# Performance work log

Measured on AMD Instinct MI355X. Metric: run time of the kernel, lower is better.

The kernel has to match this reference:

```python
import jax, jax.numpy as jnp
import numpy as np

B, D, I = 16384, 2048, 2048


def setup_inputs() -> dict:
    key = jax.random.key(0)
    kx, kh, kw = jax.random.split(key, 3)
    x = jax.random.normal(kx, (B, I), dtype=jnp.float32)
    h = jax.random.normal(kh, (B, D), dtype=jnp.float32)
    # input projection weight (Linear, no bias): [d_model, inpt_size]
    W_ih = jax.random.normal(kw, (D, I), dtype=jnp.float32) * 0.02
    # orthogonal-ish hidden transition (torch uses an SVD-orthogonal block),
    # well-conditioned so the inverse is exact and stable
    rng = np.random.default_rng(0)
    q, _ = np.linalg.qr(rng.standard_normal((D, D)).astype(np.float64))
    W_hh = jnp.asarray(q, dtype=jnp.float32)
    W_inv = jnp.asarray(np.linalg.inv(q), dtype=jnp.float32)  # buffer self.inv
    return {"x": x, "h": h, "W_ih": W_ih, "W_hh": W_hh, "W_inv": W_inv}


def reference(x, h, W_ih, W_hh, W_inv):
    # outs = inpt_linear(x) : [B, D]
    outs = jnp.einsum("bi,di->bd", x, W_ih)
    not_trig = outs[..., -1] >= -1.0          # [B]
    h_last = h[..., -1]                        # [B]
    m_fwd = ((h_last > 0) & not_trig)[..., None]   # forward rotation branch
    m_inv = ((h_last < 0) & not_trig)[..., None]   # inverse rotation branch
    m_pass = (~not_trig)[..., None]                # passthrough branch
    hW = h @ W_hh   # torch.matmul(h, weight_hh) (no transpose)
    hI = h @ W_inv  # torch.matmul(h, inv)
    zero = jnp.zeros((), dtype=outs.dtype)
    return (outs
            + jnp.where(m_fwd, hW, zero)
            + jnp.where(m_inv, hI, zero)
            + jnp.where(m_pass, h, zero))
```

## Files before the change

kernel.cpp:

```cpp
#include <hip/hip_runtime.h>
#include <hip/hip_bf16.h>
#include <stdint.h>

#define B_ROWS 16384
#define DIM 2048
#define BK 64
#define NT 96

typedef float f32x4 __attribute__((ext_vector_type(4)));
typedef short bf16x8 __attribute__((ext_vector_type(8)));
using u16 = unsigned short;
using u32 = unsigned int;

__device__ __forceinline__ u32 pack_bf2(float a, float b) {
  __hip_bfloat162 t = __float22bfloat162_rn(float2{a, b});
  union { __hip_bfloat162 b2; u32 u; } cv;
  cv.b2 = t;
  return cv.u;
}

__device__ __forceinline__ u16 f2bf_rne(float f) {
  union { float f; u32 u; } v;
  v.f = f;
  u32 u = v.u;
  u32 r = u + 0x7FFFu + ((u >> 16) & 1u);
  return (u16)(r >> 16);
}

__device__ __forceinline__ void gload16(const void* g, void* l) {
  __builtin_amdgcn_global_load_lds(
      (const __attribute__((address_space(1))) u32*)g,
      (__attribute__((address_space(3))) u32*)l, 16, 0, 0);
}

__global__ __launch_bounds__(256) void k_prep(
    const float* __restrict__ x, const float* __restrict__ h,
    const float* __restrict__ W_ih, int* __restrict__ flags,
    u16* __restrict__ xb, u16* __restrict__ hF, u16* __restrict__ hI) {
  int row = blockIdx.x * 4 + (threadIdx.x >> 6);
  int lane = threadIdx.x & 63;
  const float* xr = x + (size_t)row * DIM;
  const float* hr = h + (size_t)row * DIM;
  const float* wr = W_ih + (size_t)(DIM - 1) * DIM;
  u16* xbr = xb + (size_t)row * DIM;
  double s = 0.0;
  u32 hp[16];
#pragma unroll
  for (int i = 0; i < 8; ++i) {
    int idx = (i * 64 + lane) * 4;
    f32x4 xv = *(const f32x4*)(xr + idx);
    f32x4 wv = *(const f32x4*)(wr + idx);
    f32x4 hv = *(const f32x4*)(hr + idx);
    s += (double)xv.x * wv.x + (double)xv.y * wv.y +
         (double)xv.z * wv.z + (double)xv.w * wv.w;
    *(uint2*)(xbr + idx) = uint2{pack_bf2(xv.x, xv.y), pack_bf2(xv.z, xv.w)};
    hp[2 * i] = pack_bf2(hv.x, hv.y);
    hp[2 * i + 1] = pack_bf2(hv.z, hv.w);
  }
#pragma unroll
  for (int off = 32; off > 0; off >>= 1) s += __shfl_xor(s, off);
  float hl = hr[DIM - 1];
  int f = (s < -1.0) ? 2 : (hl > 0.f ? 0 : (hl < 0.f ? 1 : 3));
  if (lane == 0) flags[row] = f;
  uint2 z{0u, 0u};
  u16* hFr = hF + (size_t)row * DIM;
  u16* hIr = hI + (size_t)row * DIM;
#pragma unroll
  for (int i = 0; i < 8; ++i) {
    int idx = (i * 64 + lane) * 4;
    uint2 p{hp[2 * i], hp[2 * i + 1]};
    *(uint2*)(hFr + idx) = (f == 0) ? p : z;
    *(uint2*)(hIr + idx) = (f == 1) ? p : z;
  }
}

__global__ __launch_bounds__(256) void k_flags_fb(
    const float* __restrict__ x, const float* __restrict__ h,
    const float* __restrict__ W_ih, int* __restrict__ flags) {
  int row = blockIdx.x * 4 + (threadIdx.x >> 6);
  int lane = threadIdx.x & 63;
  const float* xr = x + (size_t)row * DIM;
  const float* wr = W_ih + (size_t)(DIM - 1) * DIM;
  double s = 0.0;
#pragma unroll
  for (int i = 0; i < 8; ++i) {
    int idx = (i * 64 + lane) * 4;
    f32x4 xv = *(const f32x4*)(xr + idx);
    f32x4 wv = *(const f32x4*)(wr + idx);
    s += (double)xv.x * wv.x + (double)xv.y * wv.y +
         (double)xv.z * wv.z + (double)xv.w * wv.w;
  }
#pragma unroll
  for (int off = 32; off > 0; off >>= 1) s += __shfl_xor(s, off);
  if (lane == 0) {
    float hl = h[(size_t)row * DIM + (DIM - 1)];
    flags[row] = (s < -1.0) ? 2 : (hl > 0.f ? 0 : (hl < 0.f ? 1 : 3));
  }
}

__global__ __launch_bounds__(256) void k_convert(const float* __restrict__ src,
                                                 u16* __restrict__ dst) {
  size_t i = ((size_t)blockIdx.x * 256 + threadIdx.x) * 4;
  f32x4 v = *(const f32x4*)(src + i);
  *(uint2*)(dst + i) = uint2{pack_bf2(v.x, v.y), pack_bf2(v.z, v.w)};
}

__global__ __launch_bounds__(256) void k_transpose(const float* __restrict__ src,
                                                   u16* __restrict__ dst) {
  __shared__ float tile[32][33];
  int k0 = blockIdx.x * 32;
  int n0 = blockIdx.y * 32;
  int tx = threadIdx.x & 31;
  int ty = threadIdx.x >> 5;
#pragma unroll
  for (int i = 0; i < 4; ++i)
    tile[ty + 8 * i][tx] = src[(size_t)(k0 + ty + 8 * i) * DIM + n0 + tx];
  __syncthreads();
#pragma unroll
  for (int i = 0; i < 4; ++i)
    dst[(size_t)(n0 + ty + 8 * i) * DIM + k0 + tx] = f2bf_rne(tile[tx][ty + 8 * i]);
}

__global__ __launch_bounds__(512, 2) void k_gemm8(
    const u16* __restrict__ xb, const u16* __restrict__ hF,
    const u16* __restrict__ hI, const u16* __restrict__ Wih,
    const u16* __restrict__ WhhT, const u16* __restrict__ WinvT,
    const int* __restrict__ flags, const float* __restrict__ h,
    float* __restrict__ out) {
  __shared__ __attribute__((aligned(128))) char smem[131072];

  int o = blockIdx.x;
  int swz = (o & 7) * 64 + (o >> 3);
  int brow = (swz >> 3) * 256;
  int bcol = (swz & 7) * 256;

  int t = threadIdx.x;
  int lane = t & 63;
  int wave = t >> 6;
  int wr = wave >> 2;
  int wc = wave & 3;

  int sx16 = (((lane & 3) ^ ((lane >> 3) & 3)) << 4);
  int fA = (((lane >> 4) ^ ((lane >> 1) & 3)) << 4);
  int arowbase = wr * 128 + (lane & 15);
  int browbase = wc * 64 + (lane & 15);

  auto stage = [&](int T, int isB, int kk) {
    if (T >= NT) T -= NT;
    int seg = T >> 5;
    int kt = T & 31;
    const u16* mat = isB ? (seg == 0 ? Wih : seg == 1 ? WhhT : WinvT)
                         : (seg == 0 ? xb : seg == 1 ? hF : hI);
    int r0 = isB ? bcol : brow;
    size_t gb = (size_t)(r0 + wave * 32 + (lane >> 2)) * (DIM * 2) +
                (size_t)kt * 128 + (size_t)kk * 64 + (size_t)sx16;
    char* ldst = smem + ((T & 1) << 16) + kk * 32768 + isB * 16384 +
                 (wave * 32) * 64;
    gload16((const char*)mat + gb, ldst);
    gload16((const char*)mat + gb + (size_t)16 * (DIM * 2), ldst + 1024);
  };

  f32x4 acc[8][4] = {};
  bf16x8 aF[8], bF[4];

  stage(0, 0, 0); stage(0, 1, 0);
  stage(0, 0, 1); stage(0, 1, 1);
  stage(1, 0, 0); stage(1, 1, 0);
  asm volatile("s_waitcnt vmcnt(8)" ::: "memory");
  __builtin_amdgcn_s_barrier();

#define PHASE(KK, STT, STKK)                                                   \
  {                                                                            \
    const char* Ab_ = smem + buf + (KK) * 32768;                               \
    _Pragma("unroll") for (int m = 0; m < 4; ++m) {                            \
      aF[m] = *(const bf16x8*)(Ab_ + (arowbase + m * 16) * 64 + fA);           \
      aF[4 + m] = *(const bf16x8*)(Ab_ + (arowbase + 64 + m * 16) * 64 + fA);  \
    }                                                                          \
    _Pragma("unroll") for (int n = 0; n < 4; ++n)                              \
        bF[n] = *(const bf16x8*)(Ab_ + 16384 + (browbase + n * 16) * 64 + fA); \
    stage(STT, 0, STKK);                                                       \
    stage(STT, 1, STKK);                                                       \
    asm volatile("s_waitcnt vmcnt(8)" ::: "memory");                           \
    __builtin_amdgcn_s_barrier();                                              \
    asm volatile("s_waitcnt lgkmcnt(0)" ::: "memory");                         \
    __builtin_amdgcn_sched_barrier(0);                                         \
    __builtin_amdgcn_s_setprio(1);                                             \
    _Pragma("unroll") for (int mh = 0; mh < 2; ++mh)                           \
        _Pragma("unroll") for (int m = 0; m < 4; ++m)                          \
            _Pragma("unroll") for (int n = 0; n < 4; ++n)                      \
                acc[mh * 4 + m][n] = __builtin_amdgcn_mfma_f32_16x16x32_bf16(  \
                    aF[mh * 4 + m], bF[n], acc[mh * 4 + m][n], 0, 0, 0);       \
    __builtin_amdgcn_s_setprio(0);                                             \
  }

#pragma unroll 1
  for (int T = 0; T < NT; ++T) {
    const int buf = (T & 1) << 16;
    PHASE(0, T + 1, 1)
    PHASE(1, T + 2, 0)
  }
#undef PHASE
  asm volatile("s_waitcnt vmcnt(0)" ::: "memory");

#pragma unroll
  for (int mi = 0; mi < 8; ++mi) {
    int rbase = brow + wr * 128 + (mi >> 2) * 64 + (mi & 3) * 16 + (lane >> 4) * 4;
#pragma unroll
    for (int j = 0; j < 4; ++j) {
      int row = rbase + j;
      bool pass = (flags[row] == 2);
#pragma unroll
      for (int n = 0; n < 4; ++n) {
        int col = bcol + wc * 64 + n * 16 + (lane & 15);
        float v = acc[mi][n][j];
        if (pass) v += h[(size_t)row * DIM + col];
        out[(size_t)row * DIM + col] = v;
      }
    }
  }
}

#define BM 128
#define BN 128
__global__ __launch_bounds__(256, 2) void k_gemm_fb(
    const float* __restrict__ x, const float* __restrict__ h,
    const u16* __restrict__ Wih, const u16* __restrict__ WhhT,
    const u16* __restrict__ WinvT, const int* __restrict__ flags,
    float* __restrict__ out) {
  __shared__ char smem[(BM + BN) * BK * 2];
  char* sA = smem;
  char* sB = smem + BM * BK * 2;

  int o = blockIdx.x;
  int swz = (o & 7) * ((int)gridDim.x >> 3) + (o >> 3);
  int brow = (swz >> 4) * BM;
  int bcol = (swz & 15) * BN;

  int t = threadIdx.x;
  int lane = t & 63;
  int wave = t >> 6;
  int wrow = (wave >> 1) * 64;
  int wcol = (wave & 1) * 64;

  f32x4 acc[4][4] = {};
  int sc = t & 15;
  int sr0 = t >> 4;

  int aOff[4][2], bOff[4][2];
#pragma unroll
  for (int m = 0; m < 4; ++m)
#pragma unroll
    for (int kk = 0; kk < 2; ++kk) {
      int ar = wrow + m * 16 + (lane & 15);
      aOff[m][kk] = ar * (BK * 2) + ((kk * 64 + (lane >> 4) * 16) ^ ((ar & 7) << 4));
      int br = wcol + m * 16 + (lane & 15);
      bOff[m][kk] = br * (BK * 2) + ((kk * 64 + (lane >> 4) * 16) ^ ((br & 7) << 4));
    }

#pragma unroll 1
  for (int seg = 0; seg < 3; ++seg) {
    const float* Asrc = (seg == 0) ? x : h;
    const u16* Bsrc = (seg == 0) ? Wih : (seg == 1) ? WhhT : WinvT;
    int want = seg - 1;

    float rmask[8];
#pragma unroll
    for (int i = 0; i < 8; ++i) {
      int r = sr0 + 16 * i;
      rmask[i] = (want < 0 || flags[brow + r] == want) ? 1.f : 0.f;
    }

#pragma unroll 1
    for (int k0 = 0; k0 < DIM; k0 += BK) {
      __syncthreads();
#pragma unroll
      for (int i = 0; i < 8; ++i) {
        int r = sr0 + 16 * i;
        f32x4 v = *(const f32x4*)(Asrc + (size_t)(brow + r) * DIM + k0 + sc * 4);
        float msk = rmask[i];
        int off = r * (BK * 2) + ((sc * 8) ^ ((r & 7) << 4));
        *(uint2*)(sA + off) =
            uint2{pack_bf2(v.x * msk, v.y * msk), pack_bf2(v.z * msk, v.w * msk)};
      }
#pragma unroll
      for (int i = 0; i < 4; ++i) {
        int ch = t + 256 * i;
        int r = ch >> 3;
        int c = ch & 7;
        uint4 v = *(const uint4*)(Bsrc + (size_t)(bcol + r) * DIM + k0 + c * 8);
        int off = r * (BK * 2) + ((c * 16) ^ ((r & 7) << 4));
        *(uint4*)(sB + off) = v;
      }
      __syncthreads();
      bf16x8 aF2[4][2], bF2[4][2];
#pragma unroll
      for (int m = 0; m < 4; ++m)
#pragma unroll
        for (int kk = 0; kk < 2; ++kk) {
          aF2[m][kk] = *(const bf16x8*)(sA + aOff[m][kk]);
          bF2[m][kk] = *(const bf16x8*)(sB + bOff[m][kk]);
        }
#pragma unroll
      for (int kk = 0; kk < 2; ++kk)
#pragma unroll
        for (int m = 0; m < 4; ++m)
#pragma unroll
          for (int n = 0; n < 4; ++n)
            acc[m][n] = __builtin_amdgcn_mfma_f32_16x16x32_bf16(
                aF2[m][kk], bF2[n][kk], acc[m][n], 0, 0, 0);
    }
  }

#pragma unroll
  for (int m = 0; m < 4; ++m) {
    int rbase = brow + wrow + m * 16 + (lane >> 4) * 4;
#pragma unroll
    for (int j = 0; j < 4; ++j) {
      int row = rbase + j;
      bool pass = (flags[row] == 2);
#pragma unroll
      for (int n = 0; n < 4; ++n) {
        int col = bcol + wcol + n * 16 + (lane & 15);
        float v = acc[m][n][j];
        if (pass) v += h[(size_t)row * DIM + col];
        out[(size_t)row * DIM + col] = v;
      }
    }
  }
}

extern "C" void kernel_launch(void* const* d_in, const int* in_sizes, int n_in,
                              void* d_out, int out_size, void* d_ws, size_t ws_size,
                              hipStream_t stream) {
  const float* x = (const float*)d_in[0];
  const float* h = (const float*)d_in[1];
  const float* W_ih = (const float*)d_in[2];
  const float* W_hh = (const float*)d_in[3];
  const float* W_inv = (const float*)d_in[4];
  float* out = (float*)d_out;

  char* ws = (char*)d_ws;
  int* flags = (int*)ws;
  u16* WihB = (u16*)(ws + (64 << 10));
  u16* WhhT = WihB + (size_t)DIM * DIM;
  u16* WinvT = WhhT + (size_t)DIM * DIM;
  u16* xb = WinvT + (size_t)DIM * DIM;
  u16* hF = xb + (size_t)B_ROWS * DIM;
  u16* hI = hF + (size_t)B_ROWS * DIM;
  size_t need = (size_t)(64 << 10) + 3ull * DIM * DIM * 2 + 3ull * B_ROWS * DIM * 2;

  k_convert<<<(DIM * DIM / 4) / 256, 256, 0, stream>>>(W_ih, WihB);
  k_transpose<<<dim3(DIM / 32, DIM / 32), 256, 0, stream>>>(W_hh, WhhT);
  k_transpose<<<dim3(DIM / 32, DIM / 32), 256, 0, stream>>>(W_inv, WinvT);

  if (ws_size >= need) {
    k_prep<<<B_ROWS / 4, 256, 0, stream>>>(x, h, W_ih, flags, xb, hF, hI);
    k_gemm8<<<(B_ROWS / 256) * (DIM / 256), 512, 0, stream>>>(
        xb, hF, hI, WihB, WhhT, WinvT, flags, h, out);
  } else {
    k_flags_fb<<<B_ROWS / 4, 256, 0, stream>>>(x, h, W_ih, flags);
    k_gemm_fb<<<(B_ROWS / BM) * (DIM / BN), 256, 0, stream>>>(x, h, WihB, WhhT,
                                                              WinvT, flags, out);
  }
}
```

Before: 503.2 us.

## Double-buffer MFMA operand fragments in registers to overlap LDS reads with compute

Replaces the single aF/bF fragment set with two register sets (rfA/rfB) that alternate per half-step. Each phase now issues the LDS reads for the next phase's operands and then runs MFMAs on fragments loaded in the previous phase. The old full lgkmcnt(0) wait before the MFMAs becomes a partial lgkmcnt(12) wait, and the global-load wait is tightened to vmcnt(4) to match the new prefetch distance. The aim is to hide LDS latency behind matrix math. The cost is higher VGPR pressure, which could reduce occupancy or cause spills, plus more delicate hazard ordering between the register prefetch and the LDS buffer refills.

```diff
diff --git a/kernel.cpp b/kernel.cpp
--- a/kernel.cpp
+++ b/kernel.cpp
@@ -161,45 +161,60 @@
   };
 
   f32x4 acc[8][4] = {};
-  bf16x8 aF[8], bF[4];
+  bf16x8 rfA[12], rfB[12];
 
   stage(0, 0, 0); stage(0, 1, 0);
   stage(0, 0, 1); stage(0, 1, 1);
   stage(1, 0, 0); stage(1, 1, 0);
-  asm volatile("s_waitcnt vmcnt(8)" ::: "memory");
+  asm volatile("s_waitcnt vmcnt(4)" ::: "memory");
   __builtin_amdgcn_s_barrier();
-
-#define PHASE(KK, STT, STKK)                                                   \
+#pragma unroll
+  for (int m = 0; m < 4; ++m) {
+    rfA[m] = *(const bf16x8*)(smem + (arowbase + m * 16) * 64 + fA);
+    rfA[4 + m] = *(const bf16x8*)(smem + (arowbase + 64 + m * 16) * 64 + fA);
+  }
+#pragma unroll
+  for (int n = 0; n < 4; ++n)
+    rfB[8 + n] = rfA[8 + n] = *(const bf16x8*)(smem + 16384 +
+                                               (browbase + n * 16) * 64 + fA);
+#pragma unroll
+  for (int n = 0; n < 4; ++n)
+    rfA[8 + n] = *(const bf16x8*)(smem + 16384 + (browbase + n * 16) * 64 + fA);
+
+#define PHASEBODY(RFUSE, RFLOAD, NB, ST1, SKK)                                 \
   {                                                                            \
-    const char* Ab_ = smem + buf + (KK) * 32768;                               \
+    const char* nb_ = (NB);                                                    \
     _Pragma("unroll") for (int m = 0; m < 4; ++m) {                            \
-      aF[m] = *(const bf16x8*)(Ab_ + (arowbase + m * 16) * 64 + fA);           \
-      aF[4 + m] = *(const bf16x8*)(Ab_ + (arowbase + 64 + m * 16) * 64 + fA);  \
+      RFLOAD[m] = *(const bf16x8*)(nb_ + (arowbase + m * 16) * 64 + fA);       \
+      RFLOAD[4 + m] =                                                          \
+          *(const bf16x8*)(nb_ + (arowbase + 64 + m * 16) * 64 + fA);          \
     }                                                                          \
     _Pragma("unroll") for (int n = 0; n < 4; ++n)                              \
-        bF[n] = *(const bf16x8*)(Ab_ + 16384 + (browbase + n * 16) * 64 + fA); \
-    stage(STT, 0, STKK);                                                       \
-    stage(STT, 1, STKK);                                                       \
-    asm volatile("s_waitcnt vmcnt(8)" ::: "memory");                           \
+        RFLOAD[8 + n] =                                                        \
+            *(const bf16x8*)(nb_ + 16384 + (browbase + n * 16) * 64 + fA);     \
+    stage(ST1, 0, SKK);                                                        \
+    stage(ST1, 1, SKK);                                                        \
+    asm volatile("s_waitcnt lgkmcnt(12)" ::: "memory");                        \
+    asm volatile("s_waitcnt vmcnt(4)" ::: "memory");                           \
     __builtin_amdgcn_s_barrier();                                              \
-    asm volatile("s_waitcnt lgkmcnt(0)" ::: "memory");                         \
     __builtin_amdgcn_sched_barrier(0);                                         \
     __builtin_amdgcn_s_setprio(1);                                             \
     _Pragma("unroll") for (int mh = 0; mh < 2; ++mh)                           \
         _Pragma("unroll") for (int m = 0; m < 4; ++m)                          \
             _Pragma("unroll") for (int n = 0; n < 4; ++n)                      \
                 acc[mh * 4 + m][n] = __builtin_amdgcn_mfma_f32_16x16x32_bf16(  \
-                    aF[mh * 4 + m], bF[n], acc[mh * 4 + m][n], 0, 0, 0);       \
+                    RFUSE[mh * 4 + m], RFUSE[8 + n], acc[mh * 4 + m][n],       \
+                    0, 0, 0);                                                  \
     __builtin_amdgcn_s_setprio(0);                                             \
   }
 
 #pragma unroll 1
   for (int T = 0; T < NT; ++T) {
-    const int buf = (T & 1) << 16;
-    PHASE(0, T + 1, 1)
-    PHASE(1, T + 2, 0)
-  }
-#undef PHASE
+    const int b = (T & 1) << 16;
+    PHASEBODY(rfA, rfB, smem + b + 32768, T + 1, 1)
+    PHASEBODY(rfB, rfA, smem + (b ^ 65536), T + 2, 0)
+  }
+#undef PHASEBODY
   asm volatile("s_waitcnt vmcnt(0)" ::: "memory");
 
 #pragma unroll
```

Result: slower. 517.1 us (+2.8%).

## Sort rows by branch flag so each GEMM tile computes only its needed matmul

Applied to the files above, without the earlier changes.

Rows are grouped by branch (forward, inverse, passthrough) using a single-block scan that builds a permutation. Each group is padded to 256-row tiles and packed into bf16 buffers. Each GEMM tile then runs K=4096 (x·Wih plus h·Whh or h·Winv) or only K=2048 for passthrough tiles, instead of always running K=6144 with zeroed h copies. The cost is extra kernels (flags, a serial scan, a permute gather), padding waste, and scattered output writes through the permutation.

```diff
diff --git a/kernel.cpp b/kernel.cpp
--- a/kernel.cpp
+++ b/kernel.cpp
@@ -5,7 +5,7 @@
 #define B_ROWS 16384
 #define DIM 2048
 #define BK 64
-#define NT 96
+#define MAXPR 17152
 
 typedef float f32x4 __attribute__((ext_vector_type(4)));
 typedef short bf16x8 __attribute__((ext_vector_type(8)));
@@ -33,48 +33,7 @@
       (__attribute__((address_space(3))) u32*)l, 16, 0, 0);
 }
 
-__global__ __launch_bounds__(256) void k_prep(
-    const float* __restrict__ x, const float* __restrict__ h,
-    const float* __restrict__ W_ih, int* __restrict__ flags,
-    u16* __restrict__ xb, u16* __restrict__ hF, u16* __restrict__ hI) {
-  int row = blockIdx.x * 4 + (threadIdx.x >> 6);
-  int lane = threadIdx.x & 63;
-  const float* xr = x + (size_t)row * DIM;
-  const float* hr = h + (size_t)row * DIM;
-  const float* wr = W_ih + (size_t)(DIM - 1) * DIM;
-  u16* xbr = xb + (size_t)row * DIM;
-  double s = 0.0;
-  u32 hp[16];
-#pragma unroll
-  for (int i = 0; i < 8; ++i) {
-    int idx = (i * 64 + lane) * 4;
-    f32x4 xv = *(const f32x4*)(xr + idx);
-    f32x4 wv = *(const f32x4*)(wr + idx);
-    f32x4 hv = *(const f32x4*)(hr + idx);
-    s += (double)xv.x * wv.x + (double)xv.y * wv.y +
-         (double)xv.z * wv.z + (double)xv.w * wv.w;
-    *(uint2*)(xbr + idx) = uint2{pack_bf2(xv.x, xv.y), pack_bf2(xv.z, xv.w)};
-    hp[2 * i] = pack_bf2(hv.x, hv.y);
-    hp[2 * i + 1] = pack_bf2(hv.z, hv.w);
-  }
-#pragma unroll
-  for (int off = 32; off > 0; off >>= 1) s += __shfl_xor(s, off);
-  float hl = hr[DIM - 1];
-  int f = (s < -1.0) ? 2 : (hl > 0.f ? 0 : (hl < 0.f ? 1 : 3));
-  if (lane == 0) flags[row] = f;
-  uint2 z{0u, 0u};
-  u16* hFr = hF + (size_t)row * DIM;
-  u16* hIr = hI + (size_t)row * DIM;
-#pragma unroll
-  for (int i = 0; i < 8; ++i) {
-    int idx = (i * 64 + lane) * 4;
-    uint2 p{hp[2 * i], hp[2 * i + 1]};
-    *(uint2*)(hFr + idx) = (f == 0) ? p : z;
-    *(uint2*)(hIr + idx) = (f == 1) ? p : z;
-  }
-}
-
-__global__ __launch_bounds__(256) void k_flags_fb(
+__global__ __launch_bounds__(256) void k_flags(
     const float* __restrict__ x, const float* __restrict__ h,
     const float* __restrict__ W_ih, int* __restrict__ flags) {
   int row = blockIdx.x * 4 + (threadIdx.x >> 6);
@@ -98,6 +57,82 @@
   }
 }
 
+__global__ __launch_bounds__(256) void k_scan(const int* __restrict__ flags,
+                                              int* __restrict__ iperm,
+                                              int* __restrict__ meta) {
+  __shared__ int sF[257], sI[257], sP[257];
+  int t = threadIdx.x;
+  int cF = 0, cI = 0, cP = 0;
+  for (int i = 0; i < 64; ++i) {
+    int f = flags[t * 64 + i];
+    cF += (f == 0); cI += (f == 1); cP += (f >= 2);
+  }
+  sF[t + 1] = cF; sI[t + 1] = cI; sP[t + 1] = cP;
+  for (int i = t; i < MAXPR; i += 256) iperm[i] = -1;
+  __syncthreads();
+  if (t == 0) {
+    sF[0] = sI[0] = sP[0] = 0;
+    for (int i = 1; i <= 256; ++i) {
+      sF[i] += sF[i - 1]; sI[i] += sI[i - 1]; sP[i] += sP[i - 1];
+    }
+  }
+  __syncthreads();
+  int totF = sF[256], totI = sI[256], totP = sP[256];
+  int padF = (totF + 255) & ~255;
+  int padI = (totI + 255) & ~255;
+  int rowsFI = padF + padI;
+  int nrows = rowsFI + totP;
+  if (t == 0) {
+    meta[0] = (nrows + 255) >> 8;
+    meta[1] = rowsFI >> 8;
+    meta[2] = rowsFI;
+    meta[3] = padF;
+  }
+  int oF = sF[t], oI = padF + sI[t], oP = rowsFI + sP[t];
+  for (int i = 0; i < 64; ++i) {
+    int r = t * 64 + i;
+    int f = flags[r];
+    if (f == 0) iperm[oF++] = r;
+    else if (f == 1) iperm[oI++] = r;
+    else iperm[oP++] = r;
+  }
+}
+
+__global__ __launch_bounds__(256) void k_permute(
+    const float* __restrict__ x, const float* __restrict__ h,
+    const int* __restrict__ iperm, const int* __restrict__ meta,
+    u16* __restrict__ xP, u16* __restrict__ hP) {
+  int p = blockIdx.x * 4 + (threadIdx.x >> 6);
+  int lane = threadIdx.x & 63;
+  int rowsFI = meta[2];
+  int orig = iperm[p];
+  u16* xpr = xP + (size_t)p * DIM;
+  u16* hpr = hP + (size_t)p * DIM;
+  bool doH = p < rowsFI;
+  if (orig >= 0) {
+    const float* xr = x + (size_t)orig * DIM;
+    const float* hr = h + (size_t)orig * DIM;
+#pragma unroll
+    for (int i = 0; i < 8; ++i) {
+      int idx = (i * 64 + lane) * 4;
+      f32x4 xv = *(const f32x4*)(xr + idx);
+      *(uint2*)(xpr + idx) = uint2{pack_bf2(xv.x, xv.y), pack_bf2(xv.z, xv.w)};
+      if (doH) {
+        f32x4 hv = *(const f32x4*)(hr + idx);
+        *(uint2*)(hpr + idx) = uint2{pack_bf2(hv.x, hv.y), pack_bf2(hv.z, hv.w)};
+      }
+    }
+  } else {
+    uint2 z{0u, 0u};
+#pragma unroll
+    for (int i = 0; i < 8; ++i) {
+      int idx = (i * 64 + lane) * 4;
+      *(uint2*)(xpr + idx) = z;
+      if (doH) *(uint2*)(hpr + idx) = z;
+    }
+  }
+}
+
 __global__ __launch_bounds__(256) void k_convert(const float* __restrict__ src,
                                                  u16* __restrict__ dst) {
   size_t i = ((size_t)blockIdx.x * 256 + threadIdx.x) * 4;
@@ -122,17 +157,25 @@
 }
 
 __global__ __launch_bounds__(512, 2) void k_gemm8(
-    const u16* __restrict__ xb, const u16* __restrict__ hF,
-    const u16* __restrict__ hI, const u16* __restrict__ Wih,
-    const u16* __restrict__ WhhT, const u16* __restrict__ WinvT,
-    const int* __restrict__ flags, const float* __restrict__ h,
-    float* __restrict__ out) {
+    const u16* __restrict__ xP, const u16* __restrict__ hP,
+    const u16* __restrict__ Wih, const u16* __restrict__ WhhT,
+    const u16* __restrict__ WinvT, const int* __restrict__ iperm,
+    const int* __restrict__ flags, const int* __restrict__ meta,
+    const float* __restrict__ h, float* __restrict__ out) {
   __shared__ __attribute__((aligned(128))) char smem[131072];
 
   int o = blockIdx.x;
-  int swz = (o & 7) * 64 + (o >> 3);
-  int brow = (swz >> 3) * 256;
+  int swz = (o & 7) * 67 + (o >> 3);
+  int rt = swz >> 3;
   int bcol = (swz & 7) * 256;
+  int brow = rt * 256;
+
+  int nrt = meta[0];
+  int tilesFI = meta[1];
+  int tilesF = meta[3] >> 8;
+  if (rt >= nrt) return;
+  const int NTb = (rt < tilesFI) ? 64 : 32;
+  const u16* Bh = (rt < tilesF) ? WhhT : WinvT;
 
   int t = threadIdx.x;
   int lane = t & 63;
@@ -146,12 +189,13 @@
   int browbase = wc * 64 + (lane & 15);
 
   auto stage = [&](int T, int isB, int kk) {
-    if (T >= NT) T -= NT;
-    int seg = T >> 5;
+    if (T >= NTb) T -= NTb;
+    int s = T >> 5;
     int kt = T & 31;
-    const u16* mat = isB ? (seg == 0 ? Wih : seg == 1 ? WhhT : WinvT)
-                         : (seg == 0 ? xb : seg == 1 ? hF : hI);
-    int r0 = isB ? bcol : brow;
+    const u16* mat;
+    int r0;
+    if (isB) { mat = s ? Bh : Wih; r0 = bcol; }
+    else     { mat = s ? hP : xP; r0 = brow; }
     size_t gb = (size_t)(r0 + wave * 32 + (lane >> 2)) * (DIM * 2) +
                 (size_t)kt * 128 + (size_t)kk * 64 + (size_t)sx16;
     char* ldst = smem + ((T & 1) << 16) + kk * 32768 + isB * 16384 +
@@ -194,7 +238,7 @@
   }
 
 #pragma unroll 1
-  for (int T = 0; T < NT; ++T) {
+  for (int T = 0; T < NTb; ++T) {
     const int buf = (T & 1) << 16;
     PHASE(0, T + 1, 1)
     PHASE(1, T + 2, 0)
@@ -204,17 +248,20 @@
 
 #pragma unroll
   for (int mi = 0; mi < 8; ++mi) {
-    int rbase = brow + wr * 128 + (mi >> 2) * 64 + (mi & 3) * 16 + (lane >> 4) * 4;
+    int pbase = brow + wr * 128 + (mi >> 2) * 64 + (mi & 3) * 16 + (lane >> 4) * 4;
 #pragma unroll
     for (int j = 0; j < 4; ++j) {
-      int row = rbase + j;
-      bool pass = (flags[row] == 2);
-#pragma unroll
-      for (int n = 0; n < 4; ++n) {
-        int col = bcol + wc * 64 + n * 16 + (lane & 15);
-        float v = acc[mi][n][j];
-        if (pass) v += h[(size_t)row * DIM + col];
-        out[(size_t)row * DIM + col] = v;
+      int p = pbase + j;
+      int orig = iperm[p];
+      if (orig >= 0) {
+        bool pass = (flags[orig] == 2);
+#pragma unroll
+        for (int n = 0; n < 4; ++n) {
+          int col = bcol + wc * 64 + n * 16 + (lane & 15);
+          float v = acc[mi][n][j];
+          if (pass) v += h[(size_t)orig * DIM + col];
+          out[(size_t)orig * DIM + col] = v;
+        }
       }
     }
   }
@@ -341,24 +388,26 @@
 
   char* ws = (char*)d_ws;
   int* flags = (int*)ws;
-  u16* WihB = (u16*)(ws + (64 << 10));
+  int* meta = (int*)(ws + 65536);
+  int* iperm = (int*)(ws + 65536 + 256);
+  u16* WihB = (u16*)(ws + 139264);
   u16* WhhT = WihB + (size_t)DIM * DIM;
   u16* WinvT = WhhT + (size_t)DIM * DIM;
-  u16* xb = WinvT + (size_t)DIM * DIM;
-  u16* hF = xb + (size_t)B_ROWS * DIM;
-  u16* hI = hF + (size_t)B_ROWS * DIM;
-  size_t need = (size_t)(64 << 10) + 3ull * DIM * DIM * 2 + 3ull * B_ROWS * DIM * 2;
+  u16* xP = WinvT + (size_t)DIM * DIM;
+  u16* hP = xP + (size_t)MAXPR * DIM;
+  size_t need = 139264 + 3ull * DIM * DIM * 2 + 2ull * MAXPR * DIM * 2;
 
   k_convert<<<(DIM * DIM / 4) / 256, 256, 0, stream>>>(W_ih, WihB);
   k_transpose<<<dim3(DIM / 32, DIM / 32), 256, 0, stream>>>(W_hh, WhhT);
   k_transpose<<<dim3(DIM / 32, DIM / 32), 256, 0, stream>>>(W_inv, WinvT);
+  k_flags<<<B_ROWS / 4, 256, 0, stream>>>(x, h, W_ih, flags);
 
   if (ws_size >= need) {
-    k_prep<<<B_ROWS / 4, 256, 0, stream>>>(x, h, W_ih, flags, xb, hF, hI);
-    k_gemm8<<<(B_ROWS / 256) * (DIM / 256), 512, 0, stream>>>(
-        xb, hF, hI, WihB, WhhT, WinvT, flags, h, out);
+    k_scan<<<1, 256, 0, stream>>>(flags, iperm, meta);
+    k_permute<<<MAXPR / 4, 256, 0, stream>>>(x, h, iperm, meta, xP, hP);
+    k_gemm8<<<67 * 8, 512, 0, stream>>>(xP, hP, WihB, WhhT, WinvT, iperm,
+                                        flags, meta, h, out);
   } else {
-    k_flags_fb<<<B_ROWS / 4, 256, 0, stream>>>(x, h, W_ih, flags);
     k_gemm_fb<<<(B_ROWS / BM) * (DIM / BN), 256, 0, stream>>>(x, h, WihB, WhhT,
                                                               WinvT, flags, out);
   }
```

Result: no change. 505.1 us (+0.4%).
